# Kernel tuning notes

Measured on AMD Instinct MI355X. Metric: run time of the kernel, lower is better.

Reference implementation:

```python
import jax, jax.numpy as jnp
import numpy as np

N_NODES = 50000
N_EDGES = 800000
IN_FEATS = 96
HIDDEN = 96
OUT_FEATS = 8


def setup_inputs() -> dict:
    key = jax.random.key(0)
    k = jax.random.split(key, 10)
    features = jax.random.normal(k[0], (N_NODES, IN_FEATS), dtype=jnp.float32)
    src = jax.random.randint(k[1], (N_EDGES,), 0, N_NODES, dtype=jnp.int32)
    dst = jax.random.randint(k[2], (N_EDGES,), 0, N_NODES, dtype=jnp.int32)
    # DGL GraphConv weights: shape (in, out), xavier-uniform; bias zeros (we use small randn for nontrivial grads)
    def glorot(kk, fan_in, fan_out):
        lim = np.sqrt(6.0 / (fan_in + fan_out))
        return jax.random.uniform(kk, (fan_in, fan_out), jnp.float32, -lim, lim)
    W1 = glorot(k[3], IN_FEATS, HIDDEN)
    b1 = jnp.zeros((HIDDEN,), jnp.float32)
    W2 = glorot(k[4], HIDDEN, HIDDEN)
    b2 = jnp.zeros((HIDDEN,), jnp.float32)
    # torch Linear readout: weight [out, in], bias [out]
    Wr = glorot(k[5], OUT_FEATS, HIDDEN)
    br = jnp.zeros((OUT_FEATS,), jnp.float32)
    return {"features": features, "src": src, "dst": dst,
            "W1": W1, "b1": b1, "W2": W2, "b2": b2, "Wr": Wr, "br": br}


def _degree_norms(src, dst, n_nodes):
    ones = jnp.ones(src.shape[0], jnp.float32)
    deg_out = jax.ops.segment_sum(ones, src, num_segments=n_nodes)
    deg_in = jax.ops.segment_sum(ones, dst, num_segments=n_nodes)
    norm_out = jnp.clip(deg_out, 1.0, None) ** -0.5  # D_out^{-1/2}
    norm_in = jnp.clip(deg_in, 1.0, None) ** -0.5    # D_in^{-1/2}
    return norm_out, norm_in


def _graph_conv(x, src, dst, norm_out, norm_in, W, b):
    # DGL GraphConv, norm='both': scale src feats, sum-aggregate over edges,
    # scale by in-degree norm, dense transform + bias.
    x = x * norm_out[:, None]
    msgs = x[src]                                           # [E, d] gather
    agg = jax.ops.segment_sum(msgs, dst, num_segments=x.shape[0])  # [N, d] scatter-add
    agg = agg * norm_in[:, None]
    return agg @ W + b


def reference(features, src, dst, W1, b1, W2, b2, Wr, br):
    n = features.shape[0]
    norm_out, norm_in = _degree_norms(src, dst, n)
    x = jax.nn.relu(_graph_conv(features, src, dst, norm_out, norm_in, W1, b1))
    x = _graph_conv(x, src, dst, norm_out, norm_in, W2, b2)
    hg = jnp.mean(x, axis=0, keepdims=True)  # [1, hidden]
    return hg @ Wr.T + br                    # [1, out_feats]
```

## Files before the change

### kernel.cpp

```cpp
#include <hip/hip_runtime.h>


constexpr int NN = 50000;
constexpr int NE = 800000;
constexpr int NB = 196;
constexpr int CAP = 6144;

constexpr int OFF_SVEC     = 0;
constexpr int OFF_BCURD    = 256;
constexpr int OFF_BCURS    = 3392;
constexpr int OFF_NORM_OUT = 6528;
constexpr int OFF_NORM_IN  = 56528;
constexpr int OFF_CW       = 106528;
constexpr int OFF_ROW_PTR  = 156528;
constexpr int OFF_EDGE_SRC = 206532;
constexpr int OFF_PD       = 606532;
constexpr int OFF_PS       = 1810756;
constexpr int OFF_YP       = 606532;
constexpr size_t ZERO_BYTES = (size_t)(OFF_NORM_OUT) * 4;

__global__ __launch_bounds__(256)
void k_part(const int* __restrict__ src, const int* __restrict__ dst,
            int* __restrict__ bcur_d, int* __restrict__ bcur_s,
            int* __restrict__ pd, int* __restrict__ ps) {
  __shared__ int hd[256], hs[256], gd[256], gs[256];
  __shared__ int ldx[256], cur[256], scn[256];
  __shared__ int stage[2048];
  __shared__ unsigned char stageB[2048];
  const int t = threadIdx.x;
  hd[t] = 0; hs[t] = 0;
  __syncthreads();
  const int e0 = blockIdx.x * 2048;
  int s_[8], d_[8];
#pragma unroll
  for (int i = 0; i < 8; ++i) {
    int e = e0 + i * 256 + t;
    bool v = e < NE;
    s_[i] = v ? src[e] : -1;
    d_[i] = v ? dst[e] : -1;
    if (v) { atomicAdd(&hd[d_[i] >> 8], 1); atomicAdd(&hs[s_[i] >> 8], 1); }
  }
  __syncthreads();
  if (t < NB) {
    int c = hd[t];
    gd[t] = c ? (t * CAP + atomicAdd(&bcur_d[t * 16], c)) : 0;
    c = hs[t];
    gs[t] = c ? (t * CAP + atomicAdd(&bcur_s[t * 16], c)) : 0;
  }

  scn[t] = hd[t];
  __syncthreads();
  for (int off = 1; off < 256; off <<= 1) {
    int u = (t >= off) ? scn[t - off] : 0;
    __syncthreads();
    scn[t] += u;
    __syncthreads();
  }
  ldx[t] = scn[t] - hd[t];
  cur[t] = scn[t] - hd[t];
  const int totd = scn[255];
  __syncthreads();
#pragma unroll
  for (int i = 0; i < 8; ++i) {
    if (d_[i] >= 0) {
      int B = d_[i] >> 8;
      int p = atomicAdd(&cur[B], 1);
      stage[p] = (s_[i] << 8) | (d_[i] & 255);
      stageB[p] = (unsigned char)B;
    }
  }
  __syncthreads();
  for (int j = t; j < totd; j += 256) {
    int B = stageB[j];
    pd[gd[B] + (j - ldx[B])] = stage[j];
  }
  __syncthreads();

  scn[t] = hs[t];
  __syncthreads();
  for (int off = 1; off < 256; off <<= 1) {
    int u = (t >= off) ? scn[t - off] : 0;
    __syncthreads();
    scn[t] += u;
    __syncthreads();
  }
  ldx[t] = scn[t] - hs[t];
  cur[t] = scn[t] - hs[t];
  const int tots = scn[255];
  __syncthreads();
#pragma unroll
  for (int i = 0; i < 8; ++i) {
    if (s_[i] >= 0) {
      int B = s_[i] >> 8;
      int p = atomicAdd(&cur[B], 1);
      stage[p] = (d_[i] << 8) | (s_[i] & 255);
      stageB[p] = (unsigned char)B;
    }
  }
  __syncthreads();
  for (int j = t; j < tots; j += 256) {
    int B = stageB[j];
    ps[gs[B] + (j - ldx[B])] = stage[j];
  }
}

__global__ __launch_bounds__(256)
void k_csr(const int* __restrict__ pd, const int* __restrict__ bcur_d,
           int* __restrict__ row_ptr, float* __restrict__ norm_in,
           unsigned short* __restrict__ edge_src) {
  __shared__ int pe_s[CAP];
  __shared__ int hist[256], cur[256], sc[256];
  const int t = threadIdx.x, b = blockIdx.x;
  hist[t] = 0;
  __syncthreads();
  const int cnt = bcur_d[b * 16];
  const int* pe = pd + b * CAP;
  for (int i = t; i < cnt; i += 256) {
    int p = pe[i];
    pe_s[i] = p;
    atomicAdd(&hist[p & 255], 1);
  }

  sc[t] = (t < b) ? bcur_d[t * 16] : 0;
  __syncthreads();
  for (int s = 128; s > 0; s >>= 1) {
    if (t < s) sc[t] += sc[t + s];
    __syncthreads();
  }
  const int base0 = sc[0];
  __syncthreads();

  int h = hist[t];
  sc[t] = h;
  __syncthreads();
  for (int off = 1; off < 256; off <<= 1) {
    int u = (t >= off) ? sc[t - off] : 0;
    __syncthreads();
    sc[t] += u;
    __syncthreads();
  }
  int excl = base0 + sc[t] - h;
  int n = b * 256 + t;
  if (n < NN) {
    row_ptr[n] = excl;
    norm_in[n] = 1.0f / sqrtf((float)max(h, 1));
  }
  cur[t] = excl;
  __syncthreads();
  if (b == NB - 1 && t == 0) row_ptr[NN] = base0 + cnt;

  for (int i = t; i < cnt; i += 256) {
    int p = pe_s[i];
    int pos = atomicAdd(&cur[p & 255], 1);
    edge_src[pos] = (unsigned short)(p >> 8);
  }
}

__global__ __launch_bounds__(256)
void k_bin_src(const int* __restrict__ ps, const int* __restrict__ bcur_s,
               const float* __restrict__ norm_in,
               float* __restrict__ norm_out, float* __restrict__ cw) {
  __shared__ int dout[256];
  __shared__ float craw[256];
  const int t = threadIdx.x, b = blockIdx.x;
  dout[t] = 0; craw[t] = 0.f;
  __syncthreads();
  const int cnt = bcur_s[b * 16];
  const int* pe = ps + b * CAP;
  for (int i = t; i < cnt; i += 256) {
    int p = pe[i];
    atomicAdd(&dout[p & 255], 1);
    atomicAdd(&craw[p & 255], norm_in[p >> 8]);
  }
  __syncthreads();
  int n = b * 256 + t;
  if (n < NN) {
    float no = 1.0f / sqrtf((float)max(dout[t], 1));
    norm_out[n] = no;
    cw[n] = no * craw[t];
  }
}

__global__ __launch_bounds__(256, 4)
void k_xform(const float* __restrict__ feats, const float* __restrict__ norm_out,
             const float* __restrict__ W1, float* __restrict__ YP) {
  __shared__ float XT[96][68];
  __shared__ float W1c[32][96];
  const int t = threadIdx.x;
  const int nb = blockIdx.x * 64;

  const float4* f4 = (const float4*)feats;
#pragma unroll
  for (int i = 0; i < 6; ++i) {
    int idx4 = i * 256 + t;
    int n = idx4 / 24;
    int kq = idx4 % 24;
    int ng = nb + n;
    float4 v = make_float4(0.f, 0.f, 0.f, 0.f);
    float no = 0.f;
    if (ng < NN) { v = f4[(size_t)ng * 24 + kq]; no = norm_out[ng]; }
    XT[kq * 4 + 0][n] = v.x * no;
    XT[kq * 4 + 1][n] = v.y * no;
    XT[kq * 4 + 2][n] = v.z * no;
    XT[kq * 4 + 3][n] = v.w * no;
  }
  __syncthreads();

  const int tn = t & 7;
  const int tm = t >> 3;
  float acc0[12], acc1[12];
#pragma unroll
  for (int c = 0; c < 12; ++c) { acc0[c] = 0.f; acc1[c] = 0.f; }

  for (int kb = 0; kb < 3; ++kb) {
    const float4* Wg = (const float4*)(W1 + kb * 32 * 96);
#pragma unroll
    for (int i = 0; i < 3; ++i) {
      int j = i * 256 + t;
      *(float4*)&W1c[j / 24][(j % 24) * 4] = Wg[j];
    }
    __syncthreads();
#pragma unroll
    for (int kk = 0; kk < 32; ++kk) {
      int k = kb * 32 + kk;
      float2 x = *(const float2*)&XT[k][2 * tm];
      float4 w0 = *(const float4*)&W1c[kk][12 * tn];
      float4 w1 = *(const float4*)&W1c[kk][12 * tn + 4];
      float4 w2 = *(const float4*)&W1c[kk][12 * tn + 8];
      const float w[12] = {w0.x, w0.y, w0.z, w0.w, w1.x, w1.y, w1.z, w1.w,
                           w2.x, w2.y, w2.z, w2.w};
#pragma unroll
      for (int c = 0; c < 12; ++c) {
        acc0[c] = fmaf(x.x, w[c], acc0[c]);
        acc1[c] = fmaf(x.y, w[c], acc1[c]);
      }
    }
    __syncthreads();
  }

  int n0 = nb + 2 * tm;
  if (n0 < NN) {
    float4* yp = (float4*)(YP + ((size_t)tn * NN + n0) * 12);
    yp[0] = make_float4(acc0[0], acc0[1], acc0[2], acc0[3]);
    yp[1] = make_float4(acc0[4], acc0[5], acc0[6], acc0[7]);
    yp[2] = make_float4(acc0[8], acc0[9], acc0[10], acc0[11]);
  }
  if (n0 + 1 < NN) {
    float4* yp = (float4*)(YP + ((size_t)tn * NN + n0 + 1) * 12);
    yp[0] = make_float4(acc1[0], acc1[1], acc1[2], acc1[3]);
    yp[1] = make_float4(acc1[4], acc1[5], acc1[6], acc1[7]);
    yp[2] = make_float4(acc1[8], acc1[9], acc1[10], acc1[11]);
  }
}

__global__ __launch_bounds__(256, 6)
void k_agg(const float* __restrict__ YP,
           const float* __restrict__ norm_in, const float* __restrict__ cw,
           const int* __restrict__ row_ptr, const unsigned short* __restrict__ edge_src,
           const float* __restrict__ b1, float* __restrict__ svec) {
  __shared__ float red[12];
  const int tid = threadIdx.x;
  if (tid < 12) red[tid] = 0.f;
  __syncthreads();

  const int panel = blockIdx.x & 7;
  const int bp    = blockIdx.x >> 3;
  const int g = tid >> 5, l = tid & 31;
  const int ei = l / 3;
  const int q4 = (l - 3 * ei) * 4;
  const bool act = (l < 24);

  const float* Yp = YP + (size_t)panel * NN * 12;
  float4 b4 = make_float4(0.f, 0.f, 0.f, 0.f);
  if (l < 3) b4 = ((const float4*)b1)[3 * panel + l];

  float a0 = 0.f, a1 = 0.f, a2 = 0.f, a3 = 0.f;

  const int gid = bp * 8 + g;
  for (int n = gid; n < NN; n += 4096) {
    const int m = n + 2048;
    const bool hb = (m < NN);
    int e1a = row_ptr[n + 1], basea = row_ptr[n];
    int e1b = 0, baseb = 0;
    if (hb) { e1b = row_ptr[m + 1]; baseb = row_ptr[m]; }
    float va0 = 0.f, va1 = 0.f, va2 = 0.f, va3 = 0.f;
    float vb0 = 0.f, vb1 = 0.f, vb2 = 0.f, vb3 = 0.f;

    while (basea < e1a || baseb < e1b) {
      int cnta = min(32, e1a - basea);
      int cntb = min(32, e1b - baseb);
      int esa = 0, esb = 0;
      if (basea + l < e1a) esa = edge_src[basea + l] * 12;
      if (baseb + l < e1b) esb = edge_src[baseb + l] * 12;

      if (cnta > 0) {
        int s0 = __shfl(esa, ei, 32);
        float4 f0 = make_float4(0.f, 0.f, 0.f, 0.f);
        if (act && ei < cnta) f0 = *(const float4*)(Yp + s0 + q4);
        if (cnta > 8) {
          int s1 = __shfl(esa, 8 + ei, 32);
          float4 f1 = make_float4(0.f, 0.f, 0.f, 0.f);
          if (act && 8 + ei < cnta) f1 = *(const float4*)(Yp + s1 + q4);
          f0.x += f1.x; f0.y += f1.y; f0.z += f1.z; f0.w += f1.w;
        }
        if (cnta > 16) {
          int s2 = __shfl(esa, 16 + ei, 32);
          int s3 = __shfl(esa, 24 + ei, 32);
          float4 f2 = make_float4(0.f, 0.f, 0.f, 0.f), f3 = f2;
          if (act && 16 + ei < cnta) f2 = *(const float4*)(Yp + s2 + q4);
          if (act && 24 + ei < cnta) f3 = *(const float4*)(Yp + s3 + q4);
          f0.x += f2.x + f3.x; f0.y += f2.y + f3.y;
          f0.z += f2.z + f3.z; f0.w += f2.w + f3.w;
        }
        va0 += f0.x; va1 += f0.y; va2 += f0.z; va3 += f0.w;
      }
      if (cntb > 0) {
        int s0 = __shfl(esb, ei, 32);
        float4 f0 = make_float4(0.f, 0.f, 0.f, 0.f);
        if (act && ei < cntb) f0 = *(const float4*)(Yp + s0 + q4);
        if (cntb > 8) {
          int s1 = __shfl(esb, 8 + ei, 32);
          float4 f1 = make_float4(0.f, 0.f, 0.f, 0.f);
          if (act && 8 + ei < cntb) f1 = *(const float4*)(Yp + s1 + q4);
          f0.x += f1.x; f0.y += f1.y; f0.z += f1.z; f0.w += f1.w;
        }
        if (cntb > 16) {
          int s2 = __shfl(esb, 16 + ei, 32);
          int s3 = __shfl(esb, 24 + ei, 32);
          float4 f2 = make_float4(0.f, 0.f, 0.f, 0.f), f3 = f2;
          if (act && 16 + ei < cntb) f2 = *(const float4*)(Yp + s2 + q4);
          if (act && 24 + ei < cntb) f3 = *(const float4*)(Yp + s3 + q4);
          f0.x += f2.x + f3.x; f0.y += f2.y + f3.y;
          f0.z += f2.z + f3.z; f0.w += f2.w + f3.w;
        }
        vb0 += f0.x; vb1 += f0.y; vb2 += f0.z; vb3 += f0.w;
      }
      basea += 32; baseb += 32;
    }

    va0 += __shfl(va0, l + 12, 32); va1 += __shfl(va1, l + 12, 32);
    va2 += __shfl(va2, l + 12, 32); va3 += __shfl(va3, l + 12, 32);
    va0 += __shfl(va0, l + 6, 32);  va1 += __shfl(va1, l + 6, 32);
    va2 += __shfl(va2, l + 6, 32);  va3 += __shfl(va3, l + 6, 32);
    va0 += __shfl(va0, l + 3, 32);  va1 += __shfl(va1, l + 3, 32);
    va2 += __shfl(va2, l + 3, 32);  va3 += __shfl(va3, l + 3, 32);

    vb0 += __shfl(vb0, l + 12, 32); vb1 += __shfl(vb1, l + 12, 32);
    vb2 += __shfl(vb2, l + 12, 32); vb3 += __shfl(vb3, l + 12, 32);
    vb0 += __shfl(vb0, l + 6, 32);  vb1 += __shfl(vb1, l + 6, 32);
    vb2 += __shfl(vb2, l + 6, 32);  vb3 += __shfl(vb3, l + 6, 32);
    vb0 += __shfl(vb0, l + 3, 32);  vb1 += __shfl(vb1, l + 3, 32);
    vb2 += __shfl(vb2, l + 3, 32);  vb3 += __shfl(vb3, l + 3, 32);

    if (l < 3) {
      float ni = norm_in[n], c = cw[n];
      a0 += c * fmaxf(fmaf(ni, va0, b4.x), 0.f);
      a1 += c * fmaxf(fmaf(ni, va1, b4.y), 0.f);
      a2 += c * fmaxf(fmaf(ni, va2, b4.z), 0.f);
      a3 += c * fmaxf(fmaf(ni, va3, b4.w), 0.f);
      if (hb) {
        float nib = norm_in[m], cb = cw[m];
        a0 += cb * fmaxf(fmaf(nib, vb0, b4.x), 0.f);
        a1 += cb * fmaxf(fmaf(nib, vb1, b4.y), 0.f);
        a2 += cb * fmaxf(fmaf(nib, vb2, b4.z), 0.f);
        a3 += cb * fmaxf(fmaf(nib, vb3, b4.w), 0.f);
      }
    }
  }

  if (l < 3) {
    atomicAdd(&red[4 * l + 0], a0);
    atomicAdd(&red[4 * l + 1], a1);
    atomicAdd(&red[4 * l + 2], a2);
    atomicAdd(&red[4 * l + 3], a3);
  }
  __syncthreads();
  if (tid < 12) atomicAdd(&svec[12 * panel + tid], red[tid]);
}

__global__ void k_final(const float* __restrict__ svec,
                        const float* __restrict__ W2, const float* __restrict__ b2,
                        const float* __restrict__ Wr, const float* __restrict__ br,
                        float* __restrict__ out) {
  __shared__ float hg[96];
  int j = threadIdx.x;
  if (j < 96) {
    float acc = b2[j];
    const float invN = 1.0f / (float)NN;
    for (int k = 0; k < 96; ++k)
      acc = fmaf(svec[k] * invN, W2[k * 96 + j], acc);
    hg[j] = acc;
  }
  __syncthreads();
  if (j < 8) {
    float acc = br[j];
    for (int k = 0; k < 96; ++k)
      acc = fmaf(hg[k], Wr[j * 96 + k], acc);
    out[j] = acc;
  }
}

extern "C" void kernel_launch(void* const* d_in, const int* in_sizes, int n_in,
                              void* d_out, int out_size, void* d_ws, size_t ws_size,
                              hipStream_t stream) {
  const float* feats = (const float*)d_in[0];
  const int*   src   = (const int*)d_in[1];
  const int*   dst   = (const int*)d_in[2];
  const float* W1    = (const float*)d_in[3];
  const float* b1    = (const float*)d_in[4];
  const float* W2    = (const float*)d_in[5];
  const float* b2    = (const float*)d_in[6];
  const float* Wr    = (const float*)d_in[7];
  const float* br    = (const float*)d_in[8];
  float* out = (float*)d_out;

  int*   wsi      = (int*)d_ws;
  float* wsf      = (float*)d_ws;
  float* svec     = wsf + OFF_SVEC;
  int*   bcur_d   = wsi + OFF_BCURD;
  int*   bcur_s   = wsi + OFF_BCURS;
  float* norm_out = wsf + OFF_NORM_OUT;
  float* norm_in  = wsf + OFF_NORM_IN;
  float* cw       = wsf + OFF_CW;
  int*   row_ptr  = wsi + OFF_ROW_PTR;
  unsigned short* edge_src = (unsigned short*)(wsi + OFF_EDGE_SRC);
  int*   pd       = wsi + OFF_PD;
  int*   ps       = wsi + OFF_PS;
  float* YP       = wsf + OFF_YP;

  hipMemsetAsync(d_ws, 0, ZERO_BYTES, stream);

  k_part<<<(NE + 2047) / 2048, 256, 0, stream>>>(src, dst, bcur_d, bcur_s, pd, ps);
  k_csr<<<NB, 256, 0, stream>>>(pd, bcur_d, row_ptr, norm_in, edge_src);
  k_bin_src<<<NB, 256, 0, stream>>>(ps, bcur_s, norm_in, norm_out, cw);
  k_xform<<<(NN + 63) / 64, 256, 0, stream>>>(feats, norm_out, W1, YP);
  k_agg<<<2048, 256, 0, stream>>>(YP, norm_in, cw, row_ptr, edge_src, b1, svec);
  k_final<<<1, 128, 0, stream>>>(svec, W2, b2, Wr, br, out);
}
```

Before: 208.5 us.

## Split CSR build into histogram and fused placement/src-binning kernel

The CSR kernel is split into a histogram/scan kernel and a second pass. That second pass places edges into edge_src and, in the same launch, runs the source-degree binning as a second set of blocks. This shrinks the large shared-memory staging buffer and lets placement and norm_out/cw computation run concurrently across 392 blocks instead of two serialized 196-block kernels. In exchange, the dst partition is read twice from global memory.

```diff
diff --git a/kernel.cpp b/kernel.cpp
--- a/kernel.cpp
+++ b/kernel.cpp
@@ -105,21 +105,15 @@
 }
 
 __global__ __launch_bounds__(256)
-void k_csr(const int* __restrict__ pd, const int* __restrict__ bcur_d,
-           int* __restrict__ row_ptr, float* __restrict__ norm_in,
-           unsigned short* __restrict__ edge_src) {
-  __shared__ int pe_s[CAP];
-  __shared__ int hist[256], cur[256], sc[256];
+void k_hist(const int* __restrict__ pd, const int* __restrict__ bcur_d,
+            int* __restrict__ row_ptr, float* __restrict__ norm_in) {
+  __shared__ int hist[256], sc[256];
   const int t = threadIdx.x, b = blockIdx.x;
   hist[t] = 0;
   __syncthreads();
   const int cnt = bcur_d[b * 16];
   const int* pe = pd + b * CAP;
-  for (int i = t; i < cnt; i += 256) {
-    int p = pe[i];
-    pe_s[i] = p;
-    atomicAdd(&hist[p & 255], 1);
-  }
+  for (int i = t; i < cnt; i += 256) atomicAdd(&hist[pe[i] & 255], 1);
 
   sc[t] = (t < b) ? bcur_d[t * 16] : 0;
   __syncthreads();
@@ -145,39 +139,48 @@
     row_ptr[n] = excl;
     norm_in[n] = 1.0f / sqrtf((float)max(h, 1));
   }
-  cur[t] = excl;
-  __syncthreads();
   if (b == NB - 1 && t == 0) row_ptr[NN] = base0 + cnt;
-
-  for (int i = t; i < cnt; i += 256) {
-    int p = pe_s[i];
-    int pos = atomicAdd(&cur[p & 255], 1);
-    edge_src[pos] = (unsigned short)(p >> 8);
-  }
 }
 
 __global__ __launch_bounds__(256)
-void k_bin_src(const int* __restrict__ ps, const int* __restrict__ bcur_s,
-               const float* __restrict__ norm_in,
-               float* __restrict__ norm_out, float* __restrict__ cw) {
-  __shared__ int dout[256];
-  __shared__ float craw[256];
-  const int t = threadIdx.x, b = blockIdx.x;
-  dout[t] = 0; craw[t] = 0.f;
-  __syncthreads();
-  const int cnt = bcur_s[b * 16];
-  const int* pe = ps + b * CAP;
-  for (int i = t; i < cnt; i += 256) {
-    int p = pe[i];
-    atomicAdd(&dout[p & 255], 1);
-    atomicAdd(&craw[p & 255], norm_in[p >> 8]);
-  }
-  __syncthreads();
-  int n = b * 256 + t;
-  if (n < NN) {
-    float no = 1.0f / sqrtf((float)max(dout[t], 1));
-    norm_out[n] = no;
-    cw[n] = no * craw[t];
+void k_place_bin(const int* __restrict__ pd, const int* __restrict__ ps,
+                 const int* __restrict__ bcur_d, const int* __restrict__ bcur_s,
+                 const int* __restrict__ row_ptr, const float* __restrict__ norm_in,
+                 unsigned short* __restrict__ edge_src,
+                 float* __restrict__ norm_out, float* __restrict__ cw) {
+  __shared__ int ibuf[256];
+  __shared__ float fbuf[256];
+  const int t = threadIdx.x, bb = blockIdx.x;
+  if (bb < NB) {
+    const int b = bb;
+    int n = b * 256 + t;
+    ibuf[t] = (n < NN) ? row_ptr[n] : 0;
+    __syncthreads();
+    const int cnt = bcur_d[b * 16];
+    const int* pe = pd + b * CAP;
+    for (int i = t; i < cnt; i += 256) {
+      int p = pe[i];
+      int pos = atomicAdd(&ibuf[p & 255], 1);
+      edge_src[pos] = (unsigned short)(p >> 8);
+    }
+  } else {
+    const int b = bb - NB;
+    ibuf[t] = 0; fbuf[t] = 0.f;
+    __syncthreads();
+    const int cnt = bcur_s[b * 16];
+    const int* pe = ps + b * CAP;
+    for (int i = t; i < cnt; i += 256) {
+      int p = pe[i];
+      atomicAdd(&ibuf[p & 255], 1);
+      atomicAdd(&fbuf[p & 255], norm_in[p >> 8]);
+    }
+    __syncthreads();
+    int n = b * 256 + t;
+    if (n < NN) {
+      float no = 1.0f / sqrtf((float)max(ibuf[t], 1));
+      norm_out[n] = no;
+      cw[n] = no * fbuf[t];
+    }
   }
 }
 
@@ -431,8 +434,9 @@
   hipMemsetAsync(d_ws, 0, ZERO_BYTES, stream);
 
   k_part<<<(NE + 2047) / 2048, 256, 0, stream>>>(src, dst, bcur_d, bcur_s, pd, ps);
-  k_csr<<<NB, 256, 0, stream>>>(pd, bcur_d, row_ptr, norm_in, edge_src);
-  k_bin_src<<<NB, 256, 0, stream>>>(ps, bcur_s, norm_in, norm_out, cw);
+  k_hist<<<NB, 256, 0, stream>>>(pd, bcur_d, row_ptr, norm_in);
+  k_place_bin<<<2 * NB, 256, 0, stream>>>(pd, ps, bcur_d, bcur_s, row_ptr,
+                                          norm_in, edge_src, norm_out, cw);
   k_xform<<<(NN + 63) / 64, 256, 0, stream>>>(feats, norm_out, W1, YP);
   k_agg<<<2048, 256, 0, stream>>>(YP, norm_in, cw, row_ptr, edge_src, b1, svec);
   k_final<<<1, 128, 0, stream>>>(svec, W2, b2, Wr, br, out);
```

After: 204.9 us, median of 2. No clear change (-1.7%).

## Fuse partition, CSR build and source binning into one cooperative kernel

Applied to the files above, without the earlier changes.

Merges the three preprocessing kernels into a single cooperative launch that uses grid-wide syncs between phases, and runs source-side binning concurrently with the edge_src scatter. The intent is to remove two kernel launch boundaries and their idle gaps. The CSR phase no longer stages edges in shared memory, so it reads pd from global twice, and grid.sync adds its own overhead. It also depends on all 392 blocks being co-resident.

```diff
diff --git a/kernel.cpp b/kernel.cpp
--- a/kernel.cpp
+++ b/kernel.cpp
@@ -1,10 +1,15 @@
 #include <hip/hip_runtime.h>
+#include <hip/hip_cooperative_groups.h>
+
+namespace cg = cooperative_groups;
 
 
 constexpr int NN = 50000;
 constexpr int NE = 800000;
 constexpr int NB = 196;
 constexpr int CAP = 6144;
+constexpr int NCHUNK = (NE + 2047) / 2048;
+constexpr int GRID_PRE = 2 * NB;
 
 constexpr int OFF_SVEC     = 0;
 constexpr int OFF_BCURD    = 256;
@@ -20,164 +25,163 @@
 constexpr size_t ZERO_BYTES = (size_t)(OFF_NORM_OUT) * 4;
 
 __global__ __launch_bounds__(256)
-void k_part(const int* __restrict__ src, const int* __restrict__ dst,
-            int* __restrict__ bcur_d, int* __restrict__ bcur_s,
-            int* __restrict__ pd, int* __restrict__ ps) {
+void k_pre(const int* __restrict__ src, const int* __restrict__ dst,
+           int* __restrict__ bcur_d, int* __restrict__ bcur_s,
+           int* __restrict__ pd, int* __restrict__ ps,
+           int* __restrict__ row_ptr, float* __restrict__ norm_in,
+           unsigned short* __restrict__ edge_src,
+           float* __restrict__ norm_out, float* __restrict__ cw) {
+  cg::grid_group grid = cg::this_grid();
   __shared__ int hd[256], hs[256], gd[256], gs[256];
   __shared__ int ldx[256], cur[256], scn[256];
   __shared__ int stage[2048];
   __shared__ unsigned char stageB[2048];
+  __shared__ float fbuf[256];
   const int t = threadIdx.x;
-  hd[t] = 0; hs[t] = 0;
-  __syncthreads();
-  const int e0 = blockIdx.x * 2048;
-  int s_[8], d_[8];
-#pragma unroll
-  for (int i = 0; i < 8; ++i) {
-    int e = e0 + i * 256 + t;
-    bool v = e < NE;
-    s_[i] = v ? src[e] : -1;
-    d_[i] = v ? dst[e] : -1;
-    if (v) { atomicAdd(&hd[d_[i] >> 8], 1); atomicAdd(&hs[s_[i] >> 8], 1); }
-  }
-  __syncthreads();
-  if (t < NB) {
-    int c = hd[t];
-    gd[t] = c ? (t * CAP + atomicAdd(&bcur_d[t * 16], c)) : 0;
-    c = hs[t];
-    gs[t] = c ? (t * CAP + atomicAdd(&bcur_s[t * 16], c)) : 0;
-  }
-
-  scn[t] = hd[t];
-  __syncthreads();
-  for (int off = 1; off < 256; off <<= 1) {
-    int u = (t >= off) ? scn[t - off] : 0;
-    __syncthreads();
-    scn[t] += u;
-    __syncthreads();
-  }
-  ldx[t] = scn[t] - hd[t];
-  cur[t] = scn[t] - hd[t];
-  const int totd = scn[255];
-  __syncthreads();
-#pragma unroll
-  for (int i = 0; i < 8; ++i) {
-    if (d_[i] >= 0) {
-      int B = d_[i] >> 8;
-      int p = atomicAdd(&cur[B], 1);
-      stage[p] = (s_[i] << 8) | (d_[i] & 255);
-      stageB[p] = (unsigned char)B;
-    }
-  }
-  __syncthreads();
-  for (int j = t; j < totd; j += 256) {
-    int B = stageB[j];
-    pd[gd[B] + (j - ldx[B])] = stage[j];
-  }
-  __syncthreads();
-
-  scn[t] = hs[t];
-  __syncthreads();
-  for (int off = 1; off < 256; off <<= 1) {
-    int u = (t >= off) ? scn[t - off] : 0;
-    __syncthreads();
-    scn[t] += u;
-    __syncthreads();
-  }
-  ldx[t] = scn[t] - hs[t];
-  cur[t] = scn[t] - hs[t];
-  const int tots = scn[255];
-  __syncthreads();
-#pragma unroll
-  for (int i = 0; i < 8; ++i) {
-    if (s_[i] >= 0) {
-      int B = s_[i] >> 8;
-      int p = atomicAdd(&cur[B], 1);
-      stage[p] = (d_[i] << 8) | (s_[i] & 255);
-      stageB[p] = (unsigned char)B;
-    }
-  }
-  __syncthreads();
-  for (int j = t; j < tots; j += 256) {
-    int B = stageB[j];
-    ps[gs[B] + (j - ldx[B])] = stage[j];
-  }
-}
-
-__global__ __launch_bounds__(256)
-void k_csr(const int* __restrict__ pd, const int* __restrict__ bcur_d,
-           int* __restrict__ row_ptr, float* __restrict__ norm_in,
-           unsigned short* __restrict__ edge_src) {
-  __shared__ int pe_s[CAP];
-  __shared__ int hist[256], cur[256], sc[256];
-  const int t = threadIdx.x, b = blockIdx.x;
-  hist[t] = 0;
-  __syncthreads();
-  const int cnt = bcur_d[b * 16];
-  const int* pe = pd + b * CAP;
-  for (int i = t; i < cnt; i += 256) {
-    int p = pe[i];
-    pe_s[i] = p;
-    atomicAdd(&hist[p & 255], 1);
-  }
-
-  sc[t] = (t < b) ? bcur_d[t * 16] : 0;
-  __syncthreads();
-  for (int s = 128; s > 0; s >>= 1) {
-    if (t < s) sc[t] += sc[t + s];
-    __syncthreads();
-  }
-  const int base0 = sc[0];
-  __syncthreads();
-
-  int h = hist[t];
-  sc[t] = h;
-  __syncthreads();
-  for (int off = 1; off < 256; off <<= 1) {
-    int u = (t >= off) ? sc[t - off] : 0;
-    __syncthreads();
-    sc[t] += u;
-    __syncthreads();
-  }
-  int excl = base0 + sc[t] - h;
-  int n = b * 256 + t;
-  if (n < NN) {
-    row_ptr[n] = excl;
-    norm_in[n] = 1.0f / sqrtf((float)max(h, 1));
-  }
-  cur[t] = excl;
-  __syncthreads();
-  if (b == NB - 1 && t == 0) row_ptr[NN] = base0 + cnt;
-
-  for (int i = t; i < cnt; i += 256) {
-    int p = pe_s[i];
-    int pos = atomicAdd(&cur[p & 255], 1);
-    edge_src[pos] = (unsigned short)(p >> 8);
-  }
-}
-
-__global__ __launch_bounds__(256)
-void k_bin_src(const int* __restrict__ ps, const int* __restrict__ bcur_s,
-               const float* __restrict__ norm_in,
-               float* __restrict__ norm_out, float* __restrict__ cw) {
-  __shared__ int dout[256];
-  __shared__ float craw[256];
-  const int t = threadIdx.x, b = blockIdx.x;
-  dout[t] = 0; craw[t] = 0.f;
-  __syncthreads();
-  const int cnt = bcur_s[b * 16];
-  const int* pe = ps + b * CAP;
-  for (int i = t; i < cnt; i += 256) {
-    int p = pe[i];
-    atomicAdd(&dout[p & 255], 1);
-    atomicAdd(&craw[p & 255], norm_in[p >> 8]);
-  }
-  __syncthreads();
-  int n = b * 256 + t;
-  if (n < NN) {
-    float no = 1.0f / sqrtf((float)max(dout[t], 1));
-    norm_out[n] = no;
-    cw[n] = no * craw[t];
+  const int bid = blockIdx.x;
+
+  if (bid < NCHUNK) {
+    hd[t] = 0; hs[t] = 0;
+    __syncthreads();
+    const int e0 = bid * 2048;
+    int s_[8], d_[8];
+#pragma unroll
+    for (int i = 0; i < 8; ++i) {
+      int e = e0 + i * 256 + t;
+      bool v = e < NE;
+      s_[i] = v ? src[e] : -1;
+      d_[i] = v ? dst[e] : -1;
+      if (v) { atomicAdd(&hd[d_[i] >> 8], 1); atomicAdd(&hs[s_[i] >> 8], 1); }
+    }
+    __syncthreads();
+    if (t < NB) {
+      int c = hd[t];
+      gd[t] = c ? (t * CAP + atomicAdd(&bcur_d[t * 16], c)) : 0;
+      c = hs[t];
+      gs[t] = c ? (t * CAP + atomicAdd(&bcur_s[t * 16], c)) : 0;
+    }
+
+    scn[t] = hd[t];
+    __syncthreads();
+    for (int off = 1; off < 256; off <<= 1) {
+      int u = (t >= off) ? scn[t - off] : 0;
+      __syncthreads();
+      scn[t] += u;
+      __syncthreads();
+    }
+    ldx[t] = scn[t] - hd[t];
+    cur[t] = scn[t] - hd[t];
+    const int totd = scn[255];
+    __syncthreads();
+#pragma unroll
+    for (int i = 0; i < 8; ++i) {
+      if (d_[i] >= 0) {
+        int B = d_[i] >> 8;
+        int p = atomicAdd(&cur[B], 1);
+        stage[p] = (s_[i] << 8) | (d_[i] & 255);
+        stageB[p] = (unsigned char)B;
+      }
+    }
+    __syncthreads();
+    for (int j = t; j < totd; j += 256) {
+      int B = stageB[j];
+      pd[gd[B] + (j - ldx[B])] = stage[j];
+    }
+    __syncthreads();
+
+    scn[t] = hs[t];
+    __syncthreads();
+    for (int off = 1; off < 256; off <<= 1) {
+      int u = (t >= off) ? scn[t - off] : 0;
+      __syncthreads();
+      scn[t] += u;
+      __syncthreads();
+    }
+    ldx[t] = scn[t] - hs[t];
+    cur[t] = scn[t] - hs[t];
+    const int tots = scn[255];
+    __syncthreads();
+#pragma unroll
+    for (int i = 0; i < 8; ++i) {
+      if (s_[i] >= 0) {
+        int B = s_[i] >> 8;
+        int p = atomicAdd(&cur[B], 1);
+        stage[p] = (d_[i] << 8) | (s_[i] & 255);
+        stageB[p] = (unsigned char)B;
+      }
+    }
+    __syncthreads();
+    for (int j = t; j < tots; j += 256) {
+      int B = stageB[j];
+      ps[gs[B] + (j - ldx[B])] = stage[j];
+    }
+  }
+  grid.sync();
+
+  int my_excl = 0;
+  if (bid < NB) {
+    hd[t] = 0;
+    __syncthreads();
+    const int cnt = bcur_d[bid * 16];
+    const int* pe = pd + bid * CAP;
+    for (int i = t; i < cnt; i += 256) atomicAdd(&hd[pe[i] & 255], 1);
+
+    scn[t] = (t < bid) ? bcur_d[t * 16] : 0;
+    __syncthreads();
+    for (int s = 128; s > 0; s >>= 1) {
+      if (t < s) scn[t] += scn[t + s];
+      __syncthreads();
+    }
+    const int base0 = scn[0];
+    __syncthreads();
+
+    int h = hd[t];
+    scn[t] = h;
+    __syncthreads();
+    for (int off = 1; off < 256; off <<= 1) {
+      int u = (t >= off) ? scn[t - off] : 0;
+      __syncthreads();
+      scn[t] += u;
+      __syncthreads();
+    }
+    my_excl = base0 + scn[t] - h;
+    int n = bid * 256 + t;
+    if (n < NN) {
+      row_ptr[n] = my_excl;
+      norm_in[n] = 1.0f / sqrtf((float)max(h, 1));
+    }
+    if (bid == NB - 1 && t == 0) row_ptr[NN] = base0 + cnt;
+  }
+  grid.sync();
+
+  if (bid < NB) {
+    cur[t] = my_excl;
+    __syncthreads();
+    const int cnt = bcur_d[bid * 16];
+    const int* pe = pd + bid * CAP;
+    for (int i = t; i < cnt; i += 256) {
+      int p = pe[i];
+      int pos = atomicAdd(&cur[p & 255], 1);
+      edge_src[pos] = (unsigned short)(p >> 8);
+    }
+  } else if (bid < 2 * NB) {
+    const int b = bid - NB;
+    cur[t] = 0; fbuf[t] = 0.f;
+    __syncthreads();
+    const int cnt = bcur_s[b * 16];
+    const int* pe = ps + b * CAP;
+    for (int i = t; i < cnt; i += 256) {
+      int p = pe[i];
+      atomicAdd(&cur[p & 255], 1);
+      atomicAdd(&fbuf[p & 255], norm_in[p >> 8]);
+    }
+    __syncthreads();
+    int n = b * 256 + t;
+    if (n < NN) {
+      float no = 1.0f / sqrtf((float)max(cur[t], 1));
+      norm_out[n] = no;
+      cw[n] = no * fbuf[t];
+    }
   }
 }
 
@@ -430,9 +434,12 @@
 
   hipMemsetAsync(d_ws, 0, ZERO_BYTES, stream);
 
-  k_part<<<(NE + 2047) / 2048, 256, 0, stream>>>(src, dst, bcur_d, bcur_s, pd, ps);
-  k_csr<<<NB, 256, 0, stream>>>(pd, bcur_d, row_ptr, norm_in, edge_src);
-  k_bin_src<<<NB, 256, 0, stream>>>(ps, bcur_s, norm_in, norm_out, cw);
+  void* pre_args[] = {(void*)&src, (void*)&dst, (void*)&bcur_d, (void*)&bcur_s,
+                      (void*)&pd, (void*)&ps, (void*)&row_ptr, (void*)&norm_in,
+                      (void*)&edge_src, (void*)&norm_out, (void*)&cw};
+  hipLaunchCooperativeKernel((const void*)k_pre, dim3(GRID_PRE), dim3(256),
+                             pre_args, 0, stream);
+
   k_xform<<<(NN + 63) / 64, 256, 0, stream>>>(feats, norm_out, W1, YP);
   k_agg<<<2048, 256, 0, stream>>>(YP, norm_in, cw, row_ptr, edge_src, b1, svec);
   k_final<<<1, 128, 0, stream>>>(svec, W2, b2, Wr, br, out);
```

After: 320.9 us. +53.9%, slower.
